# Performance work log

Hardware: AMD Instinct MI355X
Metric: run time of the kernel (lower is better)

## Reference

```python
import jax, jax.numpy as jnp
import numpy as np

HID, HEADS, EXP = 1024, 16, 4
HEAD_DIM = HID // HEADS
EPS = 1e-5


def setup_inputs() -> dict:
    key = jax.random.key(0)
    ks = jax.random.split(key, 16)
    s = 1.0 / np.sqrt(HID)
    d = dict(
        x=jax.random.normal(ks[0], (4, 2048, HID), jnp.float32),
        norm1_g=jnp.ones((HID,), jnp.float32),
        norm1_b=jnp.zeros((HID,), jnp.float32),
        wq=jax.random.normal(ks[1], (HID, HID), jnp.float32) * s,
        bq=jnp.zeros((HID,), jnp.float32),
        wk=jax.random.normal(ks[2], (HID, HID), jnp.float32) * s,
        bk=jnp.zeros((HID,), jnp.float32),
        wv=jax.random.normal(ks[3], (HID, HID), jnp.float32) * s,
        bv=jnp.zeros((HID,), jnp.float32),
        wo=jax.random.normal(ks[4], (HID, HID), jnp.float32) * s,
        bo=jnp.zeros((HID,), jnp.float32),
        norm2_g=jnp.ones((HID,), jnp.float32),
        norm2_b=jnp.zeros((HID,), jnp.float32),
        w1=jax.random.normal(ks[5], (HID * EXP, HID), jnp.float32) * s,
        b1=jnp.zeros((HID * EXP,), jnp.float32),
        w2=jax.random.normal(ks[6], (HID, HID * EXP), jnp.float32) * (1.0 / np.sqrt(HID * EXP)),
        b2=jnp.zeros((HID,), jnp.float32),
    )
    return d


def _layernorm(x, g, b):
    mu = jnp.mean(x, axis=-1, keepdims=True)
    var = jnp.mean(jnp.square(x - mu), axis=-1, keepdims=True)
    return (x - mu) * jax.lax.rsqrt(var + EPS) * g + b


def reference(x, norm1_g, norm1_b, wq, bq, wk, bk, wv, bv, wo, bo,
              norm2_g, norm2_b, w1, b1, w2, b2):
    B, S, _ = x.shape
    h = _layernorm(x, norm1_g, norm1_b)
    q = (h @ wq.T + bq).reshape(B, S, HEADS, HEAD_DIM)
    k = (h @ wk.T + bk).reshape(B, S, HEADS, HEAD_DIM)
    v = (h @ wv.T + bv).reshape(B, S, HEADS, HEAD_DIM)
    # scores: [B, H, S, S] (materialized, matching the naive original)
    scores = jnp.einsum('bshd,bthd->bhst', q, k) / np.sqrt(HEAD_DIM)
    attn = jax.nn.softmax(scores, axis=-1)
    out = jnp.einsum('bhst,bthd->bshd', attn, v).reshape(B, S, HID)
    x = x + out @ wo.T + bo
    h = _layernorm(x, norm2_g, norm2_b)
    ffn = jax.nn.relu(h @ w1.T + b1) @ w2.T + b2
    return x + ffn
```

## Files before the change

### kernel.cpp

```cpp
#include <hip/hip_runtime.h>
#include <hip/hip_bf16.h>

#define HID   1024
#define S_LEN 2048
#define NB    4
#define M_TOK 8192
#define HEADS 16
#define DH    64
#define FFN   4096

typedef __attribute__((ext_vector_type(8))) __bf16 bf16x8;
typedef __attribute__((ext_vector_type(4))) __bf16 bf16x4;
typedef __attribute__((ext_vector_type(4))) float  f32x4;

__device__ __forceinline__ void gl_lds16(const void* g, void* l) {
  __builtin_amdgcn_global_load_lds(
      (const __attribute__((address_space(1))) void*)g,
      (__attribute__((address_space(3))) void*)l, 16, 0, 0);
}

__device__ __forceinline__ int k3f(int r) { return (r ^ (r >> 3)) & 7; }

__global__ __launch_bounds__(256)
void cast_all_kernel(const float* __restrict__ a, const float* __restrict__ b,
                     const float* __restrict__ c, const float* __restrict__ d,
                     const float* __restrict__ e, const float* __restrict__ f,
                     __bf16* __restrict__ oa, __bf16* __restrict__ ob,
                     __bf16* __restrict__ oc, __bf16* __restrict__ od,
                     __bf16* __restrict__ oe, __bf16* __restrict__ og) {
  const int blk = blockIdx.x;
  const float* src; __bf16* dst; int boff;
  if (blk < 4096) {
    const int r = blk >> 10;
    src = (r == 0) ? a : (r == 1) ? b : (r == 2) ? c : d;
    dst = (r == 0) ? oa : (r == 1) ? ob : (r == 2) ? oc : od;
    boff = blk & 1023;
  } else if (blk < 8192) { src = e; dst = oe; boff = blk - 4096; }
  else                   { src = f; dst = og; boff = blk - 8192; }
  const int i = boff * 256 + threadIdx.x;
  float4 v = reinterpret_cast<const float4*>(src)[i];
  bf16x4 o = { (__bf16)v.x, (__bf16)v.y, (__bf16)v.z, (__bf16)v.w };
  reinterpret_cast<bf16x4*>(dst)[i] = o;
}

__global__ __launch_bounds__(256)
void ln_kernel(const float* __restrict__ x, const float* __restrict__ g,
               const float* __restrict__ bb, __bf16* __restrict__ out) {
  const int row = blockIdx.x;
  const int tid = threadIdx.x;
  const float4 v = reinterpret_cast<const float4*>(x + (size_t)row * HID)[tid];
  float s  = v.x + v.y + v.z + v.w;
  float sq = v.x*v.x + v.y*v.y + v.z*v.z + v.w*v.w;
  #pragma unroll
  for (int o = 32; o > 0; o >>= 1) { s += __shfl_down(s, o); sq += __shfl_down(sq, o); }
  __shared__ float ls[4], lq[4];
  if ((tid & 63) == 0) { ls[tid >> 6] = s; lq[tid >> 6] = sq; }
  __syncthreads();
  s  = ls[0] + ls[1] + ls[2] + ls[3];
  sq = lq[0] + lq[1] + lq[2] + lq[3];
  const float mu   = s * (1.0f / HID);
  const float rstd = rsqrtf(sq * (1.0f / HID) - mu * mu + 1e-5f);
  const float4 gv = reinterpret_cast<const float4*>(g)[tid];
  const float4 bv = reinterpret_cast<const float4*>(bb)[tid];
  bf16x4 o;
  o[0] = (__bf16)((v.x - mu) * rstd * gv.x + bv.x);
  o[1] = (__bf16)((v.y - mu) * rstd * gv.y + bv.y);
  o[2] = (__bf16)((v.z - mu) * rstd * gv.z + bv.z);
  o[3] = (__bf16)((v.w - mu) * rstd * gv.w + bv.w);
  reinterpret_cast<bf16x4*>(out + (size_t)row * HID)[tid] = o;
}

template<int EPI>
__global__ __launch_bounds__(512, 2)
void gemm_bt256(const __bf16* __restrict__ A, const __bf16* __restrict__ Bw,
                const float* __restrict__ bias,
                __bf16* __restrict__ obf, __bf16* __restrict__ ob2,
                __bf16* __restrict__ ob3, int M, int N, int K) {
  __shared__ __bf16 Al[2][256 * 64];
  __shared__ __bf16 Bl[2][256 * 64];
  const int tid  = threadIdx.x;
  const int lane = tid & 63;
  const int wid  = tid >> 6;
  const int wm = wid >> 2, wn = wid & 3;
  const int q15 = lane & 15, hi = lane >> 4;
  const int nwg = gridDim.x * gridDim.y;
  const int bid = blockIdx.y * gridDim.x + blockIdx.x;
  const int swz = (bid & 7) * (nwg >> 3) + (bid >> 3);
  const long bm = (long)(swz / gridDim.x) * 256;
  const long bn = (long)(swz % gridDim.x) * 256;
  const int sr = lane >> 3, sc = lane & 7;

  f32x4 acc[8][4] = {};
  const int nk = K >> 6;

  auto stage = [&](int b, int kt) {
    const long k0 = (long)kt << 6;
    #pragma unroll
    for (int p = 0; p < 4; ++p) {
      const int row = p * 64 + wid * 8 + sr;
      gl_lds16(A + (bm + row) * (long)K + k0 + ((sc ^ k3f(row)) << 3),
               &Al[b][(p * 64 + wid * 8) * 64]);
    }
    #pragma unroll
    for (int p = 0; p < 4; ++p) {
      const int row = p * 64 + wid * 8 + sr;
      gl_lds16(Bw + (bn + row) * (long)K + k0 + ((sc ^ k3f(row)) << 3),
               &Bl[b][(p * 64 + wid * 8) * 64]);
    }
  };

  stage(0, 0);
  int cur = 0;
  for (int t = 0; t < nk; ++t) {
    __builtin_amdgcn_s_barrier();
    __builtin_amdgcn_sched_barrier(0);
    if (t + 1 < nk) {
      stage(cur ^ 1, t + 1);
      __builtin_amdgcn_sched_barrier(0);
      asm volatile("s_waitcnt vmcnt(8)" ::: "memory");
    } else {
      asm volatile("s_waitcnt vmcnt(0)" ::: "memory");
    }
    __builtin_amdgcn_sched_barrier(0);
    __builtin_amdgcn_s_barrier();
    __builtin_amdgcn_sched_barrier(0);

    const __bf16* Ab = Al[cur];
    const __bf16* Bb = Bl[cur];
    #pragma unroll
    for (int kk = 0; kk < 2; ++kk) {
      bf16x8 af[8], bfr[4];
      #pragma unroll
      for (int mt = 0; mt < 8; ++mt) {
        const int row = wm * 128 + mt * 16 + q15;
        af[mt] = *(const bf16x8*)&Ab[row * 64 + (((kk * 4 + hi) ^ k3f(row)) << 3)];
      }
      #pragma unroll
      for (int nt = 0; nt < 4; ++nt) {
        const int row = wn * 64 + nt * 16 + q15;
        bfr[nt] = *(const bf16x8*)&Bb[row * 64 + (((kk * 4 + hi) ^ k3f(row)) << 3)];
      }
      __builtin_amdgcn_s_setprio(1);
      #pragma unroll
      for (int mt = 0; mt < 8; ++mt)
        #pragma unroll
        for (int nt = 0; nt < 4; ++nt)
          acc[mt][nt] = __builtin_amdgcn_mfma_f32_16x16x32_bf16(af[mt], bfr[nt], acc[mt][nt], 0, 0, 0);
      __builtin_amdgcn_s_setprio(0);
    }
    cur ^= 1;
  }

  #pragma unroll
  for (int mt = 0; mt < 8; ++mt) {
    const long row0 = bm + wm * 128 + mt * 16 + (hi << 2);
    #pragma unroll
    for (int nt = 0; nt < 4; ++nt) {
      const long col = bn + wn * 64 + nt * 16 + q15;
      const float bsv = bias[col];
      #pragma unroll
      for (int j = 0; j < 4; ++j) {
        const float val = acc[mt][nt][j] + bsv;
        if (EPI == 1) {
          obf[(row0 + j) * (long)N + col] = (__bf16)fmaxf(val, 0.0f);
        } else {
          __bf16* dst = (col < 1024) ? obf : ((col < 2048) ? ob2 : ob3);
          dst[(row0 + j) * 1024L + (col & 1023)] = (__bf16)val;
        }
      }
    }
  }
}

__global__ __launch_bounds__(512, 2)
void gemm_btMN(const __bf16* __restrict__ A, const __bf16* __restrict__ Bw,
               const float* __restrict__ bias, const float* __restrict__ res,
               float* __restrict__ of, int M, int N, int K) {
  __shared__ __bf16 Al[2][256 * 64];
  __shared__ __bf16 Bl[2][128 * 64];
  const int tid  = threadIdx.x;
  const int lane = tid & 63;
  const int wid  = tid >> 6;
  const int wm = wid >> 1, wn = wid & 1;
  const int q15 = lane & 15, hi = lane >> 4;
  const int nwg = gridDim.x * gridDim.y;
  const int bid = blockIdx.y * gridDim.x + blockIdx.x;
  const int swz = (bid & 7) * (nwg >> 3) + (bid >> 3);
  const long bm = (long)(swz / gridDim.x) * 256;
  const long bn = (long)(swz % gridDim.x) * 128;
  const int sr = lane >> 3, sc = lane & 7;

  f32x4 acc[4][4] = {};
  const int nk = K >> 6;

  auto stage = [&](int b, int kt) {
    const long k0 = (long)kt << 6;
    #pragma unroll
    for (int p = 0; p < 4; ++p) {
      const int row = wid * 32 + p * 8 + sr;
      gl_lds16(A + (bm + row) * (long)K + k0 + ((sc ^ k3f(row)) << 3),
               &Al[b][(wid * 32 + p * 8) * 64]);
    }
    #pragma unroll
    for (int p = 0; p < 2; ++p) {
      const int row = wid * 16 + p * 8 + sr;
      gl_lds16(Bw + (bn + row) * (long)K + k0 + ((sc ^ k3f(row)) << 3),
               &Bl[b][(wid * 16 + p * 8) * 64]);
    }
  };

  stage(0, 0);
  int cur = 0;
  for (int t = 0; t < nk; ++t) {
    __builtin_amdgcn_s_barrier();
    __builtin_amdgcn_sched_barrier(0);
    if (t + 1 < nk) {
      stage(cur ^ 1, t + 1);
      __builtin_amdgcn_sched_barrier(0);
      asm volatile("s_waitcnt vmcnt(6)" ::: "memory");
    } else {
      asm volatile("s_waitcnt vmcnt(0)" ::: "memory");
    }
    __builtin_amdgcn_sched_barrier(0);
    __builtin_amdgcn_s_barrier();
    __builtin_amdgcn_sched_barrier(0);

    const __bf16* Ab = Al[cur];
    const __bf16* Bb = Bl[cur];
    #pragma unroll
    for (int kk = 0; kk < 2; ++kk) {
      bf16x8 af[4], bfr[4];
      #pragma unroll
      for (int mt = 0; mt < 4; ++mt) {
        const int row = wm * 64 + mt * 16 + q15;
        af[mt] = *(const bf16x8*)&Ab[row * 64 + (((kk * 4 + hi) ^ k3f(row)) << 3)];
      }
      #pragma unroll
      for (int nt = 0; nt < 4; ++nt) {
        const int row = wn * 64 + nt * 16 + q15;
        bfr[nt] = *(const bf16x8*)&Bb[row * 64 + (((kk * 4 + hi) ^ k3f(row)) << 3)];
      }
      __builtin_amdgcn_s_setprio(1);
      #pragma unroll
      for (int mt = 0; mt < 4; ++mt)
        #pragma unroll
        for (int nt = 0; nt < 4; ++nt)
          acc[mt][nt] = __builtin_amdgcn_mfma_f32_16x16x32_bf16(af[mt], bfr[nt], acc[mt][nt], 0, 0, 0);
      __builtin_amdgcn_s_setprio(0);
    }
    cur ^= 1;
  }

  #pragma unroll
  for (int mt = 0; mt < 4; ++mt) {
    const long row0 = bm + wm * 64 + mt * 16 + (hi << 2);
    #pragma unroll
    for (int nt = 0; nt < 4; ++nt) {
      const long col = bn + wn * 64 + nt * 16 + q15;
      const float bsv = bias[col];
      #pragma unroll
      for (int j = 0; j < 4; ++j) {
        const long idx = (row0 + j) * (long)N + col;
        of[idx] = res[idx] + acc[mt][nt][j] + bsv;
      }
    }
  }
}

__global__ __launch_bounds__(256)
void vtrans_kernel(const __bf16* __restrict__ v, __bf16* __restrict__ vt) {
  __shared__ __bf16 t[4096];
  const int tid = threadIdx.x;
  const int bh = blockIdx.y, b = bh >> 4, h = bh & 15;
  const int s0 = blockIdx.x * 64;
  const int r = tid >> 3, c8 = tid & 7;
  #pragma unroll
  for (int i = 0; i < 2; ++i) {
    const int row = i * 32 + r;
    bf16x8 val = *(const bf16x8*)(v + ((size_t)(b * S_LEN + s0 + row)) * HID + h * DH + c8 * 8);
    *(bf16x8*)&t[row * 64 + ((c8 ^ k3f(row)) << 3)] = val;
  }
  __syncthreads();
  #pragma unroll
  for (int i = 0; i < 2; ++i) {
    const int d = i * 32 + r;
    bf16x8 ovec;
    #pragma unroll
    for (int j = 0; j < 8; ++j) {
      const int s = c8 * 8 + j;
      ovec[j] = t[s * 64 + ((((d >> 3) ^ k3f(s)) << 3) | (d & 7))];
    }
    *(bf16x8*)(vt + ((size_t)(bh * 64 + d)) * S_LEN + s0 + c8 * 8) = ovec;
  }
}

__global__ __launch_bounds__(512, 6)
void attn_kernel(const __bf16* __restrict__ q, const __bf16* __restrict__ k,
                 const __bf16* __restrict__ vt, __bf16* __restrict__ o) {
  __shared__ __bf16 Kl[2][64 * 64];
  __shared__ __bf16 Vt[2][64 * 64];
  __shared__ __bf16 Pl[8 * 16 * 72];
  const int tid = threadIdx.x, lane = tid & 63, wid = tid >> 6;
  const int q15 = lane & 15, hi4 = lane >> 4;
  const int bh = blockIdx.x, b = bh >> 4, h = bh & 15;
  const size_t base = ((size_t)b * S_LEN) * HID + h * DH;
  const int q0 = blockIdx.y * 128 + wid * 16;
  const int r8 = lane >> 3, c8 = lane & 7;

  const __bf16* kfp[4][2];
  const __bf16* vfp[2][4];
  #pragma unroll
  for (int ct = 0; ct < 4; ++ct) {
    const int rk = ct * 16 + q15;
    const int k3 = k3f(rk);
    #pragma unroll
    for (int kk = 0; kk < 2; ++kk)
      kfp[ct][kk] = &Kl[0][rk * 64 + (((kk * 4 + hi4) ^ k3) << 3)];
  }
  #pragma unroll
  for (int kk = 0; kk < 2; ++kk)
    #pragma unroll
    for (int dt = 0; dt < 4; ++dt) {
      const int dv = dt * 16 + q15;
      vfp[kk][dt] = &Vt[0][dv * 64 + (((kk * 4 + hi4) ^ k3f(dv)) << 3)];
    }
  __bf16* pb = &Pl[wid * (16 * 72)];
  __bf16* pwp[4];
  const __bf16* prp[2];
  #pragma unroll
  for (int ct = 0; ct < 4; ++ct) pwp[ct] = &pb[q15 * 72 + ct * 16 + hi4 * 4];
  #pragma unroll
  for (int kk = 0; kk < 2; ++kk) prp[kk] = &pb[q15 * 72 + kk * 32 + hi4 * 8];

  const int srow = wid * 8 + r8;
  const __bf16* kp = k + base + (size_t)srow * HID + ((c8 ^ k3f(srow)) << 3);
  const __bf16* vp = vt + (size_t)bh * 64 * S_LEN + (size_t)srow * S_LEN
                        + ((c8 ^ k3f(srow)) << 3);
  __bf16* kd0 = &Kl[0][wid * 8 * 64];
  __bf16* kd1 = &Kl[1][wid * 8 * 64];
  __bf16* vd0 = &Vt[0][wid * 8 * 64];
  __bf16* vd1 = &Vt[1][wid * 8 * 64];

  bf16x8 qf[2];
  {
    const __bf16* qp = q + base + (size_t)(q0 + q15) * HID + hi4 * 8;
    #pragma unroll
    for (int kk = 0; kk < 2; ++kk) {
      bf16x8 t = *(const bf16x8*)(qp + kk * 32);
      #pragma unroll
      for (int j = 0; j < 8; ++j) t[j] = (__bf16)((float)t[j] * 0.1803368801f);
      qf[kk] = t;
    }
  }

  f32x4 oacc[4] = {};
  float lp = 0.f;

  gl_lds16(kp, kd0);  kp += 64 * HID;
  gl_lds16(vp, vd0);  vp += 64;

  for (int t = 0; t < S_LEN / 64; t += 2) {
    #pragma unroll
    for (int half = 0; half < 2; ++half) {
      const int OFF = half ? 4096 : 0;
      __builtin_amdgcn_s_barrier();
      __builtin_amdgcn_sched_barrier(0);
      if (t + half + 1 < S_LEN / 64) {
        gl_lds16(kp, half ? kd0 : kd1);  kp += 64 * HID;
        gl_lds16(vp, half ? vd0 : vd1);  vp += 64;
        __builtin_amdgcn_sched_barrier(0);
        asm volatile("s_waitcnt vmcnt(2)" ::: "memory");
      } else {
        asm volatile("s_waitcnt vmcnt(0)" ::: "memory");
      }
      __builtin_amdgcn_sched_barrier(0);
      __builtin_amdgcn_s_barrier();
      __builtin_amdgcn_sched_barrier(0);

      f32x4 sacc[4] = {};
      __builtin_amdgcn_s_setprio(1);
      #pragma unroll
      for (int ct = 0; ct < 4; ++ct)
        #pragma unroll
        for (int kk = 0; kk < 2; ++kk)
          sacc[ct] = __builtin_amdgcn_mfma_f32_16x16x32_bf16(
              *(const bf16x8*)(kfp[ct][kk] + OFF), qf[kk], sacc[ct], 0, 0, 0);
      __builtin_amdgcn_s_setprio(0);

      #pragma unroll
      for (int ct = 0; ct < 4; ++ct) {
        bf16x4 w;
        #pragma unroll
        for (int jj = 0; jj < 4; ++jj) {
          const float p = __builtin_amdgcn_exp2f(sacc[ct][jj] - 16.0f);
          lp += p;
          w[jj] = (__bf16)p;
        }
        *(bf16x4*)pwp[ct] = w;
      }

      __builtin_amdgcn_s_setprio(1);
      #pragma unroll
      for (int kk = 0; kk < 2; ++kk) {
        bf16x8 pf = *(const bf16x8*)prp[kk];
        #pragma unroll
        for (int dt = 0; dt < 4; ++dt)
          oacc[dt] = __builtin_amdgcn_mfma_f32_16x16x32_bf16(
              pf, *(const bf16x8*)(vfp[kk][dt] + OFF), oacc[dt], 0, 0, 0);
      }
      __builtin_amdgcn_s_setprio(0);
    }
  }

  float lrun = lp;
  lrun += __shfl_xor(lrun, 16);
  lrun += __shfl_xor(lrun, 32);
  const float inv = 1.0f / lrun;
  #pragma unroll
  for (int jj = 0; jj < 4; ++jj) {
    const float iO = __shfl(inv, (hi4 << 4) | (hi4 * 4 + jj));
    const size_t orow = base + (size_t)(q0 + hi4 * 4 + jj) * HID;
    #pragma unroll
    for (int dt = 0; dt < 4; ++dt)
      o[orow + dt * 16 + q15] = (__bf16)(oacc[dt][jj] * iO);
  }
}

extern "C" void kernel_launch(void* const* d_in, const int* in_sizes, int n_in,
                              void* d_out, int out_size, void* d_ws, size_t ws_size,
                              hipStream_t stream) {
  (void)in_sizes; (void)n_in; (void)out_size; (void)ws_size;
  const float* x   = (const float*)d_in[0];
  const float* n1g = (const float*)d_in[1];
  const float* n1b = (const float*)d_in[2];
  const float* wq  = (const float*)d_in[3];
  const float* bq  = (const float*)d_in[4];
  const float* wk  = (const float*)d_in[5];
  const float* bk  = (const float*)d_in[6];
  const float* wv  = (const float*)d_in[7];
  const float* bv  = (const float*)d_in[8];
  const float* wo  = (const float*)d_in[9];
  const float* bo  = (const float*)d_in[10];
  const float* n2g = (const float*)d_in[11];
  const float* n2b = (const float*)d_in[12];
  const float* w1  = (const float*)d_in[13];
  const float* b1  = (const float*)d_in[14];
  const float* w2  = (const float*)d_in[15];
  const float* b2  = (const float*)d_in[16];

  char* ws = (char*)d_ws;
  const size_t MB = 1ull << 20;
  __bf16* wq_b = (__bf16*)(ws);
  __bf16* wk_b = (__bf16*)(ws + 2 * MB);
  __bf16* wv_b = (__bf16*)(ws + 4 * MB);
  __bf16* wo_b = (__bf16*)(ws + 6 * MB);
  __bf16* w1_b = (__bf16*)(ws + 8 * MB);
  __bf16* w2_b = (__bf16*)(ws + 16 * MB);
  __bf16* h1   = (__bf16*)(ws + 24 * MB);
  __bf16* qb   = (__bf16*)(ws + 40 * MB);
  __bf16* kb   = (__bf16*)(ws + 56 * MB);
  __bf16* vb   = (__bf16*)(ws + 72 * MB);
  __bf16* vtb  = (__bf16*)(ws + 88 * MB);
  __bf16* ffn1 = (__bf16*)(ws + 56 * MB);
  float*  bqkv = (float*)(ws + 118 * MB);
  float*  x2   = (float*)(ws + 120 * MB);

  cast_all_kernel<<<12288, 256, 0, stream>>>(wq, wk, wv, wo, w1, w2,
                                             wq_b, wk_b, wv_b, wo_b, w1_b, w2_b);

  hipMemcpyAsync(bqkv,        bq, 1024 * sizeof(float), hipMemcpyDeviceToDevice, stream);
  hipMemcpyAsync(bqkv + 1024, bk, 1024 * sizeof(float), hipMemcpyDeviceToDevice, stream);
  hipMemcpyAsync(bqkv + 2048, bv, 1024 * sizeof(float), hipMemcpyDeviceToDevice, stream);

  ln_kernel<<<M_TOK, 256, 0, stream>>>(x, n1g, n1b, h1);

  dim3 gqkv(3072 / 256, M_TOK / 256);
  gemm_bt256<3><<<gqkv, 512, 0, stream>>>(h1, wq_b, bqkv, qb, kb, vb,
                                          M_TOK, 3072, HID);

  dim3 gt(S_LEN / 64, NB * HEADS);
  vtrans_kernel<<<gt, 256, 0, stream>>>(vb, vtb);

  dim3 ga(NB * HEADS, S_LEN / 128);
  attn_kernel<<<ga, 512, 0, stream>>>(qb, kb, vtb, h1);

  dim3 g1(HID / 128, M_TOK / 256);
  gemm_btMN<<<g1, 512, 0, stream>>>(h1, wo_b, bo, x, x2, M_TOK, HID, HID);

  ln_kernel<<<M_TOK, 256, 0, stream>>>(x2, n2g, n2b, qb);

  dim3 g2(FFN / 256, M_TOK / 256);
  gemm_bt256<1><<<g2, 512, 0, stream>>>(qb, w1_b, b1, ffn1, nullptr, nullptr,
                                        M_TOK, FFN, HID);

  gemm_btMN<<<g1, 512, 0, stream>>>(ffn1, w2_b, b2, x2, (float*)d_out,
                                    M_TOK, HID, FFN);
}
```

Before: 429.4 us.

## Keep attention probabilities in registers by permuting V transpose key order

The attention kernel no longer writes the exponentiated scores to shared memory and reads them back as the A operand of the PV MFMA. The S^T MFMA output is packed straight into bf16x8 registers with v_cvt_pk_bf16_f32. To make this register layout match the MFMA's expected key ordering, the V-transpose kernel now permutes key positions within each 64-key tile. Dropping the P buffer frees LDS, so the occupancy hint rises from 6 to 8 blocks. The approach depends on the permutation exactly matching the MFMA register layout, and the higher occupancy target may force register spills.

```diff
diff --git a/kernel.cpp b/kernel.cpp
--- a/kernel.cpp
+++ b/kernel.cpp
@@ -12,6 +12,7 @@
 typedef __attribute__((ext_vector_type(8))) __bf16 bf16x8;
 typedef __attribute__((ext_vector_type(4))) __bf16 bf16x4;
 typedef __attribute__((ext_vector_type(4))) float  f32x4;
+typedef __attribute__((ext_vector_type(4))) int    i32x4;
 
 __device__ __forceinline__ void gl_lds16(const void* g, void* l) {
   __builtin_amdgcn_global_load_lds(
@@ -20,6 +21,12 @@
 }
 
 __device__ __forceinline__ int k3f(int r) { return (r ^ (r >> 3)) & 7; }
+
+__device__ __forceinline__ unsigned int cvtpk(float a, float b) {
+  unsigned int d;
+  asm("v_cvt_pk_bf16_f32 %0, %1, %2" : "=v"(d) : "v"(a), "v"(b));
+  return d;
+}
 
 __global__ __launch_bounds__(256)
 void cast_all_kernel(const float* __restrict__ a, const float* __restrict__ b,
@@ -287,19 +294,19 @@
     bf16x8 ovec;
     #pragma unroll
     for (int j = 0; j < 8; ++j) {
-      const int s = c8 * 8 + j;
+      const int x = c8 * 8 + j;
+      const int s = (x & 0x20) | ((x & 4) << 2) | ((x & 0x18) >> 1) | (x & 3);
       ovec[j] = t[s * 64 + ((((d >> 3) ^ k3f(s)) << 3) | (d & 7))];
     }
     *(bf16x8*)(vt + ((size_t)(bh * 64 + d)) * S_LEN + s0 + c8 * 8) = ovec;
   }
 }
 
-__global__ __launch_bounds__(512, 6)
+__global__ __launch_bounds__(512, 8)
 void attn_kernel(const __bf16* __restrict__ q, const __bf16* __restrict__ k,
                  const __bf16* __restrict__ vt, __bf16* __restrict__ o) {
   __shared__ __bf16 Kl[2][64 * 64];
   __shared__ __bf16 Vt[2][64 * 64];
-  __shared__ __bf16 Pl[8 * 16 * 72];
   const int tid = threadIdx.x, lane = tid & 63, wid = tid >> 6;
   const int q15 = lane & 15, hi4 = lane >> 4;
   const int bh = blockIdx.x, b = bh >> 4, h = bh & 15;
@@ -324,13 +331,6 @@
       const int dv = dt * 16 + q15;
       vfp[kk][dt] = &Vt[0][dv * 64 + (((kk * 4 + hi4) ^ k3f(dv)) << 3)];
     }
-  __bf16* pb = &Pl[wid * (16 * 72)];
-  __bf16* pwp[4];
-  const __bf16* prp[2];
-  #pragma unroll
-  for (int ct = 0; ct < 4; ++ct) pwp[ct] = &pb[q15 * 72 + ct * 16 + hi4 * 4];
-  #pragma unroll
-  for (int kk = 0; kk < 2; ++kk) prp[kk] = &pb[q15 * 72 + kk * 32 + hi4 * 8];
 
   const int srow = wid * 8 + r8;
   const __bf16* kp = k + base + (size_t)srow * HID + ((c8 ^ k3f(srow)) << 3);
@@ -377,37 +377,40 @@
       __builtin_amdgcn_s_barrier();
       __builtin_amdgcn_sched_barrier(0);
 
-      f32x4 sacc[4] = {};
+      bf16x8 pa[2];
+      #pragma unroll
+      for (int pp = 0; pp < 2; ++pp) {
+        f32x4 sa = {}, sb = {};
+        __builtin_amdgcn_s_setprio(1);
+        #pragma unroll
+        for (int kk = 0; kk < 2; ++kk) {
+          sa = __builtin_amdgcn_mfma_f32_16x16x32_bf16(
+              *(const bf16x8*)(kfp[2 * pp + 0][kk] + OFF), qf[kk], sa, 0, 0, 0);
+          sb = __builtin_amdgcn_mfma_f32_16x16x32_bf16(
+              *(const bf16x8*)(kfp[2 * pp + 1][kk] + OFF), qf[kk], sb, 0, 0, 0);
+        }
+        __builtin_amdgcn_s_setprio(0);
+        float e0 = __builtin_amdgcn_exp2f(sa[0] - 16.0f);
+        float e1 = __builtin_amdgcn_exp2f(sa[1] - 16.0f);
+        float e2 = __builtin_amdgcn_exp2f(sa[2] - 16.0f);
+        float e3 = __builtin_amdgcn_exp2f(sa[3] - 16.0f);
+        float e4 = __builtin_amdgcn_exp2f(sb[0] - 16.0f);
+        float e5 = __builtin_amdgcn_exp2f(sb[1] - 16.0f);
+        float e6 = __builtin_amdgcn_exp2f(sb[2] - 16.0f);
+        float e7 = __builtin_amdgcn_exp2f(sb[3] - 16.0f);
+        lp += ((e0 + e1) + (e2 + e3)) + ((e4 + e5) + (e6 + e7));
+        i32x4 w = { (int)cvtpk(e0, e1), (int)cvtpk(e2, e3),
+                    (int)cvtpk(e4, e5), (int)cvtpk(e6, e7) };
+        pa[pp] = __builtin_bit_cast(bf16x8, w);
+      }
+
       __builtin_amdgcn_s_setprio(1);
       #pragma unroll
-      for (int ct = 0; ct < 4; ++ct)
-        #pragma unroll
-        for (int kk = 0; kk < 2; ++kk)
-          sacc[ct] = __builtin_amdgcn_mfma_f32_16x16x32_bf16(
-              *(const bf16x8*)(kfp[ct][kk] + OFF), qf[kk], sacc[ct], 0, 0, 0);
-      __builtin_amdgcn_s_setprio(0);
-
-      #pragma unroll
-      for (int ct = 0; ct < 4; ++ct) {
-        bf16x4 w;
-        #pragma unroll
-        for (int jj = 0; jj < 4; ++jj) {
-          const float p = __builtin_amdgcn_exp2f(sacc[ct][jj] - 16.0f);
-          lp += p;
-          w[jj] = (__bf16)p;
-        }
-        *(bf16x4*)pwp[ct] = w;
-      }
-
-      __builtin_amdgcn_s_setprio(1);
-      #pragma unroll
-      for (int kk = 0; kk < 2; ++kk) {
-        bf16x8 pf = *(const bf16x8*)prp[kk];
+      for (int kk = 0; kk < 2; ++kk)
         #pragma unroll
         for (int dt = 0; dt < 4; ++dt)
           oacc[dt] = __builtin_amdgcn_mfma_f32_16x16x32_bf16(
-              pf, *(const bf16x8*)(vfp[kk][dt] + OFF), oacc[dt], 0, 0, 0);
-      }
+              pa[kk], *(const bf16x8*)(vfp[kk][dt] + OFF), oacc[dt], 0, 0, 0);
       __builtin_amdgcn_s_setprio(0);
     }
   }
```

Result: slower. 526.6 us (+22.6%).
